# Kernel optimization log

Measured on AMD Instinct MI355X. Metric: run time of the kernel, lower is better.

Reference implementation:

```python
import jax, jax.numpy as jnp
import numpy as np

D_MODEL = 1024
N_HEADS = 16
D_KV = 64
INNER = N_HEADS * D_KV
NUM_BUCKETS = 32
MAX_DISTANCE = 128
B, S = 4, 2048


def _relative_position_bucket(relative_position):
    # Mirrors T5Attention._relative_position_bucket (bidirectional variant)
    num_buckets = NUM_BUCKETS // 2  # 16
    relative_buckets = (relative_position > 0).astype(jnp.int32) * num_buckets
    rp = jnp.abs(relative_position)
    max_exact = num_buckets // 2  # 8
    is_small = rp < max_exact
    # clamp to 1 before log to avoid -inf (masked out by where anyway)
    rp_large = max_exact + (
        jnp.log(jnp.maximum(rp, 1).astype(jnp.float32) / max_exact)
        / np.log(MAX_DISTANCE / max_exact)
        * (num_buckets - max_exact)
    ).astype(jnp.int32)
    rp_large = jnp.minimum(rp_large, num_buckets - 1)
    return relative_buckets + jnp.where(is_small, rp.astype(jnp.int32), rp_large)


def setup_inputs() -> dict:
    key = jax.random.key(0)
    k1, k2, k3, k4, k5, k6 = jax.random.split(key, 6)
    hidden_states = jax.random.normal(k1, (B, S, D_MODEL), dtype=jnp.float32)
    positions = jnp.arange(B * S, dtype=jnp.int64 if jax.config.jax_enable_x64 else jnp.int32).reshape(B, S)
    mask = jnp.ones((B, S), dtype=jnp.float32)
    sc = 1.0 / np.sqrt(D_MODEL)
    wq = jax.random.normal(k2, (INNER, D_MODEL), dtype=jnp.float32) * sc
    wk = jax.random.normal(k3, (INNER, D_MODEL), dtype=jnp.float32) * sc
    wv = jax.random.normal(k4, (INNER, D_MODEL), dtype=jnp.float32) * sc
    wo = jax.random.normal(k5, (D_MODEL, INNER), dtype=jnp.float32) * sc
    rel_bias = jax.random.normal(k6, (NUM_BUCKETS, N_HEADS), dtype=jnp.float32)
    return {"hidden_states": hidden_states, "positions": positions, "mask": mask,
            "wq": wq, "wk": wk, "wv": wv, "wo": wo, "rel_bias": rel_bias}


def reference(hidden_states, positions, mask, wq, wk, wv, wo, rel_bias):
    Bq, Sq, _ = hidden_states.shape

    def shape_heads(x):  # [B,S,inner] -> [B,H,S,dkv]
        return x.reshape(Bq, Sq, N_HEADS, D_KV).transpose(0, 2, 1, 3)

    # position bias: [B,H,Sq,Sk]
    rel_pos = positions[:, None, :] - positions[:, :, None]  # memory - context
    buckets = _relative_position_bucket(rel_pos)             # [B,Sq,Sk]
    position_bias = rel_bias[buckets].transpose(0, 3, 1, 2)  # [B,H,Sq,Sk]

    q = shape_heads(hidden_states @ wq.T).astype(jnp.float32)
    k = shape_heads(hidden_states @ wk.T).astype(jnp.float32)
    v = shape_heads(hidden_states @ wv.T).astype(jnp.float32)

    scores = jnp.einsum('bhqd,bhkd->bhqk', q, k)  # no 1/sqrt(d) scaling (T5)
    bias = position_bias - 1000.0 * (1.0 - mask[:, None, None, :])
    attn = jax.nn.softmax(scores + bias, axis=-1)  # dropout p=0

    ctx = jnp.einsum('bhqk,bhkd->bhqd', attn, v)
    ctx = ctx.transpose(0, 2, 1, 3).reshape(Bq, Sq, INNER).astype(hidden_states.dtype)
    return ctx @ wo.T
```

## Files before the change

kernel.cpp:

```cpp
#include <hip/hip_runtime.h>
#include <cstdint>
#include <cstddef>

#define D_MODEL 1024
#define N_HEADS 16
#define INNER   1024
#define NBATCH  4
#define SEQ     2048
#define MTOT    (NBATCH * SEQ)
#define LOG2E   1.44269504088896f
#define BSTRIDE 4352
#define MASKC   1442.695041f

typedef _Float16 f16;
typedef __attribute__((ext_vector_type(8))) _Float16 f16x8;
typedef __attribute__((ext_vector_type(4))) _Float16 f16x4;
typedef __attribute__((ext_vector_type(2))) _Float16 f16x2;
typedef __attribute__((ext_vector_type(2))) __fp16   h16x2;
typedef __attribute__((ext_vector_type(4))) float    f32x4;

__device__ __forceinline__ f16x2 cvtpk(float x, float y) {
#if __has_builtin(__builtin_amdgcn_cvt_pkrtz)
  h16x2 r = __builtin_amdgcn_cvt_pkrtz(x, y);
  return __builtin_bit_cast(f16x2, r);
#else
  f16x2 r; r[0] = (f16)x; r[1] = (f16)y; return r;
#endif
}
__device__ __forceinline__ float dot2acc(f16x2 p, float acc) {
#if __has_builtin(__builtin_amdgcn_fdot2)
  h16x2 a = __builtin_bit_cast(h16x2, p);
  h16x2 one; one[0] = (__fp16)1.0f; one[1] = (__fp16)1.0f;
  return __builtin_amdgcn_fdot2(a, one, acc, false);
#else
  return acc + (float)p[0] + (float)p[1];
#endif
}

__global__ void k_cvt(const float* __restrict__ src, f16* __restrict__ dst, int n4, float scale) {
  int i = blockIdx.x * 256 + threadIdx.x;
  if (i < n4) {
    const float4 v = reinterpret_cast<const float4*>(src)[i];
    f16x4 h;
    h[0] = (f16)(v.x * scale); h[1] = (f16)(v.y * scale);
    h[2] = (f16)(v.z * scale); h[3] = (f16)(v.w * scale);
    reinterpret_cast<f16x4*>(dst)[i] = h;
  }
}

__global__ void k_bias(const float* __restrict__ relb, float* __restrict__ biasG) {
  const int i = blockIdx.x * 256 + threadIdx.x;
  const int h = blockIdx.y;
  const int d = i - 2048;
  const int sgn = d > 0 ? 16 : 0;
  const int a = d < 0 ? -d : d;
  int bucket;
  if (a < 8) {
    bucket = a;
  } else {
    float t = logf((float)a / 8.0f);
    t = t / 2.772588722239781f;
    t = t * 8.0f;
    int lg = 8 + (int)t;
    bucket = lg < 15 ? lg : 15;
  }
  biasG[h * BSTRIDE + i] = relb[(sgn + bucket) * N_HEADS + h] * LOG2E - MASKC;
}

__device__ __forceinline__ void gload_lds16(const void* g, void* l) {
  __builtin_amdgcn_global_load_lds(
      (const __attribute__((address_space(1))) unsigned int*)g,
      (__attribute__((address_space(3))) unsigned int*)l,
      16, 0, 0);
}

template <int MODE>
__device__ __forceinline__ void gemm_body(const f16* __restrict__ A,
                                          const f16* __restrict__ W,
                                          void* __restrict__ Cp) {
  __shared__ __align__(16) f16 As[128 * 64];
  __shared__ __align__(16) f16 Bs[128 * 64];
  const int t = threadIdx.x;
  const int lane = t & 63;
  const int wid = t >> 6;
  const int wr = wid >> 1;
  const int wc = wid & 1;
  const int g = lane >> 4;
  const int lr = lane & 15;
  const int m0 = blockIdx.y * 128;
  const int n0 = blockIdx.x * 128;

  f32x4 acc[4][4] = {};
  const char* Ab = (const char*)A;
  const char* Wb = (const char*)W;

  for (int kt = 0; kt < D_MODEL / 64; ++kt) {
    const int k0 = kt * 64;
    __syncthreads();
#pragma unroll
    for (int i = 0; i < 4; ++i) {
      const int idx = i * 256 + t;
      const int row = idx >> 3;
      const int cb  = (idx & 7) * 16;
      gload_lds16(Ab + ((size_t)(m0 + row) * D_MODEL + k0) * 2 + cb, (char*)As + idx * 16);
      gload_lds16(Wb + ((size_t)(n0 + row) * D_MODEL + k0) * 2 + cb, (char*)Bs + idx * 16);
    }
    asm volatile("s_waitcnt vmcnt(0)" ::: "memory");
    __syncthreads();

    f16x8 af[4][2], bf[4][2];
#pragma unroll
    for (int mi = 0; mi < 4; ++mi)
#pragma unroll
      for (int kk = 0; kk < 2; ++kk)
        af[mi][kk] = *(const f16x8*)&As[(wr * 64 + mi * 16 + lr) * 64 + kk * 32 + g * 8];
#pragma unroll
    for (int ni = 0; ni < 4; ++ni)
#pragma unroll
      for (int kk = 0; kk < 2; ++kk)
        bf[ni][kk] = *(const f16x8*)&Bs[(wc * 64 + ni * 16 + lr) * 64 + kk * 32 + g * 8];
#pragma unroll
    for (int kk = 0; kk < 2; ++kk)
#pragma unroll
      for (int mi = 0; mi < 4; ++mi)
#pragma unroll
        for (int ni = 0; ni < 4; ++ni)
          acc[mi][ni] = __builtin_amdgcn_mfma_f32_16x16x32_f16(af[mi][kk], bf[ni][kk], acc[mi][ni], 0, 0, 0);
  }

#pragma unroll
  for (int mi = 0; mi < 4; ++mi)
#pragma unroll
    for (int ni = 0; ni < 4; ++ni) {
      const int n = n0 + wc * 64 + ni * 16 + lr;
      if (MODE == 2) {
        const int mbase = m0 + wr * 64 + mi * 16 + g * 4;
        const int b2 = mbase >> 11, s2 = mbase & (SEQ - 1);
        const int h2 = n >> 6, d2 = n & 63;
        f16x4 w;
#pragma unroll
        for (int r = 0; r < 4; ++r) w[r] = (f16)acc[mi][ni][r];
        *(f16x4*)((f16*)Cp + ((size_t)((b2 * 16 + h2) * 64 + d2) * SEQ + s2)) = w;
      } else {
#pragma unroll
        for (int r = 0; r < 4; ++r) {
          const int m = m0 + wr * 64 + mi * 16 + g * 4 + r;
          if (MODE == 1)
            ((float*)Cp)[(size_t)m * INNER + n] = acc[mi][ni][r];
          else
            ((f16*)Cp)[(size_t)m * INNER + n] = (f16)acc[mi][ni][r];
        }
      }
    }
}

__global__ __launch_bounds__(256) void k_gemm_qkv(
    const f16* __restrict__ A,
    const f16* __restrict__ Wq, const f16* __restrict__ Wk, const f16* __restrict__ Wv,
    f16* __restrict__ Cq, f16* __restrict__ Ck, f16* __restrict__ Vt) {
  if (blockIdx.z == 0)      gemm_body<0>(A, Wq, Cq);
  else if (blockIdx.z == 1) gemm_body<0>(A, Wk, Ck);
  else                      gemm_body<2>(A, Wv, Vt);
}

__global__ __launch_bounds__(256) void k_gemm_out(
    const f16* __restrict__ A, const f16* __restrict__ W, float* __restrict__ C) {
  gemm_body<1>(A, W, C);
}

__global__ __launch_bounds__(256, 4) void k_attn(
    const f16* __restrict__ Q, const f16* __restrict__ K, const f16* __restrict__ Vt,
    const float* __restrict__ biasG, const float* __restrict__ mask,
    f16* __restrict__ ctx) {
  __shared__ __align__(16) float biasT[2176];
  __shared__ __align__(16) f16 Ks[2 * 2048];
  __shared__ __align__(16) f16 Vs[2 * 2048];

  const int nb = (int)blockIdx.x;
  const int v = (nb & 7) * 128 + (nb >> 3);
  const int bh = v >> 4, qc = v & 15;
  const int b = bh >> 4, h = bh & 15;

  const int t = threadIdx.x, lane = t & 63, wid = t >> 6;
  const int g = lane >> 4, lr = lane & 15;
  const int qb = qc * 128;

  {
    const float* bgh = biasG + (size_t)h * BSTRIDE + (1921 - qb);
    for (int i = t; i < 2176; i += 256) biasT[i] = bgh[i];
  }

  const char* Kg = (const char*)K + ((size_t)(b * SEQ) * INNER + h * 64) * 2;
  const char* Vg = (const char*)Vt + ((size_t)bh * 64) * SEQ * 2;
  const float* maskB = mask + (size_t)b * SEQ;
  const int krow = t >> 3, kch = t & 7;
  const int ksrc = (kch * 16) ^ ((krow & 7) << 4);
  const int vrow = t >> 2, vch = t & 3;
  const int vsrc = (vch * 16) ^ ((vrow & 3) << 4);

  const int qw = qb + wid * 32;

  f16x8 qa[2][2];
#pragma unroll
  for (int hh = 0; hh < 2; ++hh)
#pragma unroll
    for (int kk = 0; kk < 2; ++kk)
      qa[hh][kk] = *(const f16x8*)&Q[(size_t)(b * SEQ + qw + hh * 16 + lr) * INNER + h * 64 + kk * 32 + g * 8];

  int koffs[2][2], voffs[2][4];
#pragma unroll
  for (int s = 0; s < 2; ++s) {
#pragma unroll
    for (int hf = 0; hf < 2; ++hf)
      koffs[s][hf] = (s * 16 + lr) * 128 + ((hf * 64 + g * 16) ^ ((lr & 7) << 4));
#pragma unroll
    for (int dn = 0; dn < 4; ++dn)
      voffs[s][dn] = (dn * 16 + lr) * 64 + ((s * 32 + g * 8) ^ ((lr & 3) << 4));
  }

  f32x4 o[2][4] = {};
  float mrun[2] = {-__builtin_inff(), -__builtin_inff()};
  float lsum[2] = {0.0f, 0.0f};
  const int jbase = 127 + 4 * g - wid * 32 - lr;

  gload_lds16(Kg + ((size_t)krow * INNER) * 2 + ksrc, (char*)Ks + t * 16);
  gload_lds16(Vg + ((size_t)vrow * SEQ) * 2 + vsrc,   (char*)Vs + t * 16);
  asm volatile("s_waitcnt vmcnt(0)" ::: "memory");
  __syncthreads();

#define ATTN_ITER(BUF, K0)                                                     \
  {                                                                            \
    const float4 mk0 = *(const float4*)(maskB + (K0) + 4 * g);                 \
    const float4 mk1 = *(const float4*)(maskB + (K0) + 16 + 4 * g);            \
    const int k0n_ = ((K0) + 32 < SEQ) ? (K0) + 32 : 0;                        \
    gload_lds16(Kg + ((size_t)(k0n_ + krow) * INNER) * 2 + ksrc,               \
                (char*)Ks + ((BUF) ^ 1) * 4096 + t * 16);                      \
    gload_lds16(Vg + ((size_t)vrow * SEQ + k0n_) * 2 + vsrc,                   \
                (char*)Vs + ((BUF) ^ 1) * 4096 + t * 16);                      \
    f16x8 kf[2][2];                                                            \
    _Pragma("unroll") for (int s = 0; s < 2; ++s)                              \
      _Pragma("unroll") for (int hf = 0; hf < 2; ++hf)                         \
        kf[s][hf] = *(const f16x8*)((const char*)Ks + (BUF) * 4096 + koffs[s][hf]); \
    f16x4 vf[2][4];                                                            \
    _Pragma("unroll") for (int s = 0; s < 2; ++s)                              \
      _Pragma("unroll") for (int dn = 0; dn < 4; ++dn)                         \
        vf[s][dn] = *(const f16x4*)((const char*)Vs + (BUF) * 4096 + voffs[s][dn]); \
    f32x4 sg[2][2];                                                            \
    _Pragma("unroll") for (int hh = 0; hh < 2; ++hh)                           \
      _Pragma("unroll") for (int s = 0; s < 2; ++s) {                          \
        const int jA = (K0) + s * 16 + jbase - hh * 16;                        \
        const float* mkp = (s == 0) ? (const float*)&mk0 : (const float*)&mk1; \
        f32x4 z;                                                               \
        _Pragma("unroll") for (int r = 0; r < 4; ++r)                          \
          z[r] = fmaf(mkp[r], MASKC, biasT[jA + r]);                           \
        z = __builtin_amdgcn_mfma_f32_16x16x32_f16(kf[s][0], qa[hh][0], z, 0, 0, 0); \
        z = __builtin_amdgcn_mfma_f32_16x16x32_f16(kf[s][1], qa[hh][1], z, 0, 0, 0); \
        sg[hh][s] = z;                                                         \
      }                                                                        \
    float mxA = fmaxf(fmaxf(fmaxf(sg[0][0][0], sg[0][0][1]), fmaxf(sg[0][0][2], sg[0][0][3])), \
                      fmaxf(fmaxf(sg[0][1][0], sg[0][1][1]), fmaxf(sg[0][1][2], sg[0][1][3]))); \
    float mxB = fmaxf(fmaxf(fmaxf(sg[1][0][0], sg[1][0][1]), fmaxf(sg[1][0][2], sg[1][0][3])), \
                      fmaxf(fmaxf(sg[1][1][0], sg[1][1][1]), fmaxf(sg[1][1][2], sg[1][1][3]))); \
    if (__any((mxA > mrun[0] + 11.5415603f) || (mxB > mrun[1] + 11.5415603f))) { \
      mxA = fmaxf(mxA, __shfl_xor(mxA, 16));                                   \
      mxB = fmaxf(mxB, __shfl_xor(mxB, 16));                                   \
      mxA = fmaxf(mxA, __shfl_xor(mxA, 32));                                   \
      mxB = fmaxf(mxB, __shfl_xor(mxB, 32));                                   \
      const float mnA = fmaxf(mrun[0], mxA), mnB = fmaxf(mrun[1], mxB);        \
      const float aA = __builtin_amdgcn_exp2f(mrun[0] - mnA);                  \
      const float aB = __builtin_amdgcn_exp2f(mrun[1] - mnB);                  \
      lsum[0] *= aA; lsum[1] *= aB;                                            \
      _Pragma("unroll") for (int dn = 0; dn < 4; ++dn)                         \
        _Pragma("unroll") for (int r = 0; r < 4; ++r) {                        \
          o[0][dn][r] *= aA; o[1][dn][r] *= aB;                                \
        }                                                                      \
      mrun[0] = mnA; mrun[1] = mnB;                                            \
    }                                                                          \
    f16x4 pfA[2], pfB[2];                                                      \
    _Pragma("unroll") for (int s = 0; s < 2; ++s) {                            \
      float eA[4], eB[4];                                                      \
      _Pragma("unroll") for (int r = 0; r < 4; ++r) {                          \
        eA[r] = __builtin_amdgcn_exp2f(sg[0][s][r] - mrun[0]);                 \
        eB[r] = __builtin_amdgcn_exp2f(sg[1][s][r] - mrun[1]);                 \
      }                                                                        \
      const f16x2 a0 = cvtpk(eA[0], eA[1]), a1 = cvtpk(eA[2], eA[3]);          \
      const f16x2 b0 = cvtpk(eB[0], eB[1]), b1 = cvtpk(eB[2], eB[3]);          \
      lsum[0] = dot2acc(a0, lsum[0]); lsum[0] = dot2acc(a1, lsum[0]);          \
      lsum[1] = dot2acc(b0, lsum[1]); lsum[1] = dot2acc(b1, lsum[1]);          \
      pfA[s][0] = a0[0]; pfA[s][1] = a0[1]; pfA[s][2] = a1[0]; pfA[s][3] = a1[1]; \
      pfB[s][0] = b0[0]; pfB[s][1] = b0[1]; pfB[s][2] = b1[0]; pfB[s][3] = b1[1]; \
    }                                                                          \
    _Pragma("unroll") for (int s = 0; s < 2; ++s)                              \
      _Pragma("unroll") for (int dn = 0; dn < 4; ++dn) {                       \
        o[0][dn] = __builtin_amdgcn_mfma_f32_16x16x16f16(vf[s][dn], pfA[s], o[0][dn], 0, 0, 0); \
        o[1][dn] = __builtin_amdgcn_mfma_f32_16x16x16f16(vf[s][dn], pfB[s], o[1][dn], 0, 0, 0); \
      }                                                                        \
    asm volatile("s_waitcnt vmcnt(0)" ::: "memory");                           \
    __syncthreads();                                                           \
  }

  for (int k0 = 0; k0 < SEQ; k0 += 64) {
    ATTN_ITER(0, k0)
    ATTN_ITER(1, k0 + 32)
  }

  lsum[0] += __shfl_xor(lsum[0], 16);
  lsum[1] += __shfl_xor(lsum[1], 16);
  lsum[0] += __shfl_xor(lsum[0], 32);
  lsum[1] += __shfl_xor(lsum[1], 32);

  const float invA = 1.0f / lsum[0], invB = 1.0f / lsum[1];
#pragma unroll
  for (int dn = 0; dn < 4; ++dn) {
    f16x4 wA, wB;
#pragma unroll
    for (int r = 0; r < 4; ++r) {
      wA[r] = (f16)(o[0][dn][r] * invA);
      wB[r] = (f16)(o[1][dn][r] * invB);
    }
    *(f16x4*)&ctx[(size_t)(b * SEQ + qw + lr) * INNER + h * 64 + dn * 16 + 4 * g] = wA;
    *(f16x4*)&ctx[(size_t)(b * SEQ + qw + 16 + lr) * INNER + h * 64 + dn * 16 + 4 * g] = wB;
  }
}

extern "C" void kernel_launch(void* const* d_in, const int* in_sizes, int n_in,
                              void* d_out, int out_size, void* d_ws, size_t ws_size,
                              hipStream_t stream) {
  const float* hs   = (const float*)d_in[0];
  const float* mask = (const float*)d_in[2];
  const float* wq   = (const float*)d_in[3];
  const float* wk   = (const float*)d_in[4];
  const float* wv   = (const float*)d_in[5];
  const float* wo   = (const float*)d_in[6];
  const float* relb = (const float*)d_in[7];

  char* ws = (char*)d_ws;
  const size_t SZ16 = (size_t)MTOT * INNER * 2;
  const size_t WSZ  = (size_t)INNER * D_MODEL * 2;
  f16* hs16 = (f16*)(ws);
  f16* q16  = (f16*)(ws + SZ16);
  f16* k16  = (f16*)(ws + 2 * SZ16);
  f16* vt16 = (f16*)(ws + 3 * SZ16);
  f16* wq16 = (f16*)(ws + 4 * SZ16);
  f16* wk16 = (f16*)(ws + 4 * SZ16 + WSZ);
  f16* wv16 = (f16*)(ws + 4 * SZ16 + 2 * WSZ);
  f16* wo16 = (f16*)(ws + 4 * SZ16 + 3 * WSZ);
  float* biasG = (float*)(ws + 4 * SZ16 + 4 * WSZ);

  k_cvt<<<(MTOT * INNER / 4 + 255) / 256, 256, 0, stream>>>(hs, hs16, MTOT * INNER / 4, 1.0f);
  k_cvt<<<(INNER * D_MODEL / 4 + 255) / 256, 256, 0, stream>>>(wq, wq16, INNER * D_MODEL / 4, LOG2E);
  k_cvt<<<(INNER * D_MODEL / 4 + 255) / 256, 256, 0, stream>>>(wk, wk16, INNER * D_MODEL / 4, 1.0f);
  k_cvt<<<(INNER * D_MODEL / 4 + 255) / 256, 256, 0, stream>>>(wv, wv16, INNER * D_MODEL / 4, 1.0f);
  k_cvt<<<(INNER * D_MODEL / 4 + 255) / 256, 256, 0, stream>>>(wo, wo16, INNER * D_MODEL / 4, 1.0f);

  k_bias<<<dim3(BSTRIDE / 256, N_HEADS), 256, 0, stream>>>(relb, biasG);

  k_gemm_qkv<<<dim3(INNER / 128, MTOT / 128, 3), 256, 0, stream>>>(
      hs16, wq16, wk16, wv16, q16, k16, vt16);

  k_attn<<<dim3(1024), 256, 0, stream>>>(
      q16, k16, vt16, biasG, mask, hs16);

  k_gemm_out<<<dim3(D_MODEL / 128, MTOT / 128), 256, 0, stream>>>(
      hs16, wo16, (float*)d_out);
}
```

Baseline: 255.1 us.

## Split attention work to 8 waves of 16 query rows each per block

Measured after the change: 309.5 us. 1.21x slower.

```diff
diff --git a/kernel.cpp b/kernel.cpp
--- a/kernel.cpp
+++ b/kernel.cpp
@@ -168,7 +168,7 @@
   gemm_body<1>(A, W, C);
 }
 
-__global__ __launch_bounds__(256, 4) void k_attn(
+__global__ __launch_bounds__(512, 6) void k_attn(
     const f16* __restrict__ Q, const f16* __restrict__ K, const f16* __restrict__ Vt,
     const float* __restrict__ biasG, const float* __restrict__ mask,
     f16* __restrict__ ctx) {
@@ -187,25 +187,26 @@
 
   {
     const float* bgh = biasG + (size_t)h * BSTRIDE + (1921 - qb);
-    for (int i = t; i < 2176; i += 256) biasT[i] = bgh[i];
+    for (int i = t; i < 2176; i += 512) biasT[i] = bgh[i];
   }
 
   const char* Kg = (const char*)K + ((size_t)(b * SEQ) * INNER + h * 64) * 2;
   const char* Vg = (const char*)Vt + ((size_t)bh * 64) * SEQ * 2;
   const float* maskB = mask + (size_t)b * SEQ;
-  const int krow = t >> 3, kch = t & 7;
-  const int ksrc = (kch * 16) ^ ((krow & 7) << 4);
-  const int vrow = t >> 2, vch = t & 3;
-  const int vsrc = (vch * 16) ^ ((vrow & 3) << 4);
-
-  const int qw = qb + wid * 32;
-
-  f16x8 qa[2][2];
-#pragma unroll
-  for (int hh = 0; hh < 2; ++hh)
-#pragma unroll
-    for (int kk = 0; kk < 2; ++kk)
-      qa[hh][kk] = *(const f16x8*)&Q[(size_t)(b * SEQ + qw + hh * 16 + lr) * INNER + h * 64 + kk * 32 + g * 8];
+
+  const bool isK = t < 256;
+  const int ts = t & 255;
+  const int krow = ts >> 3, kch = ts & 7;
+  const int vrow = ts >> 2, vch = ts & 3;
+  const int stsrc = isK ? ((kch * 16) ^ ((krow & 7) << 4))
+                        : ((vch * 16) ^ ((vrow & 3) << 4));
+
+  const int qw = qb + wid * 16;
+
+  f16x8 qa[2];
+#pragma unroll
+  for (int kk = 0; kk < 2; ++kk)
+    qa[kk] = *(const f16x8*)&Q[(size_t)(b * SEQ + qw + lr) * INNER + h * 64 + kk * 32 + g * 8];
 
   int koffs[2][2], voffs[2][4];
 #pragma unroll
@@ -218,13 +219,15 @@
       voffs[s][dn] = (dn * 16 + lr) * 64 + ((s * 32 + g * 8) ^ ((lr & 3) << 4));
   }
 
-  f32x4 o[2][4] = {};
-  float mrun[2] = {-__builtin_inff(), -__builtin_inff()};
-  float lsum[2] = {0.0f, 0.0f};
-  const int jbase = 127 + 4 * g - wid * 32 - lr;
-
-  gload_lds16(Kg + ((size_t)krow * INNER) * 2 + ksrc, (char*)Ks + t * 16);
-  gload_lds16(Vg + ((size_t)vrow * SEQ) * 2 + vsrc,   (char*)Vs + t * 16);
+  f32x4 o[4] = {};
+  float mrun = -__builtin_inff();
+  float lsum = 0.0f;
+  const int jbase = 127 + 4 * g - wid * 16 - lr;
+
+  if (isK)
+    gload_lds16(Kg + ((size_t)krow * INNER) * 2 + stsrc, (char*)Ks + ts * 16);
+  else
+    gload_lds16(Vg + ((size_t)vrow * SEQ) * 2 + stsrc,   (char*)Vs + ts * 16);
   asm volatile("s_waitcnt vmcnt(0)" ::: "memory");
   __syncthreads();
 
@@ -233,67 +236,53 @@
     const float4 mk0 = *(const float4*)(maskB + (K0) + 4 * g);                 \
     const float4 mk1 = *(const float4*)(maskB + (K0) + 16 + 4 * g);            \
     const int k0n_ = ((K0) + 32 < SEQ) ? (K0) + 32 : 0;                        \
-    gload_lds16(Kg + ((size_t)(k0n_ + krow) * INNER) * 2 + ksrc,               \
-                (char*)Ks + ((BUF) ^ 1) * 4096 + t * 16);                      \
-    gload_lds16(Vg + ((size_t)vrow * SEQ + k0n_) * 2 + vsrc,                   \
-                (char*)Vs + ((BUF) ^ 1) * 4096 + t * 16);                      \
+    if (isK)                                                                   \
+      gload_lds16(Kg + ((size_t)(k0n_ + krow) * INNER) * 2 + stsrc,            \
+                  (char*)Ks + ((BUF) ^ 1) * 4096 + ts * 16);                   \
+    else                                                                       \
+      gload_lds16(Vg + ((size_t)vrow * SEQ + k0n_) * 2 + stsrc,                \
+                  (char*)Vs + ((BUF) ^ 1) * 4096 + ts * 16);                   \
     f16x8 kf[2][2];                                                            \
     _Pragma("unroll") for (int s = 0; s < 2; ++s)                              \
       _Pragma("unroll") for (int hf = 0; hf < 2; ++hf)                         \
         kf[s][hf] = *(const f16x8*)((const char*)Ks + (BUF) * 4096 + koffs[s][hf]); \
-    f16x4 vf[2][4];                                                            \
-    _Pragma("unroll") for (int s = 0; s < 2; ++s)                              \
+    f32x4 sg[2];                                                               \
+    _Pragma("unroll") for (int s = 0; s < 2; ++s) {                            \
+      const int jA = (K0) + s * 16 + jbase;                                    \
+      const float* mkp = (s == 0) ? (const float*)&mk0 : (const float*)&mk1;   \
+      f32x4 z;                                                                 \
+      _Pragma("unroll") for (int r = 0; r < 4; ++r)                            \
+        z[r] = fmaf(mkp[r], MASKC, biasT[jA + r]);                             \
+      z = __builtin_amdgcn_mfma_f32_16x16x32_f16(kf[s][0], qa[0], z, 0, 0, 0); \
+      z = __builtin_amdgcn_mfma_f32_16x16x32_f16(kf[s][1], qa[1], z, 0, 0, 0); \
+      sg[s] = z;                                                               \
+    }                                                                          \
+    float mx = fmaxf(fmaxf(fmaxf(sg[0][0], sg[0][1]), fmaxf(sg[0][2], sg[0][3])), \
+                     fmaxf(fmaxf(sg[1][0], sg[1][1]), fmaxf(sg[1][2], sg[1][3]))); \
+    if (__any(mx > mrun + 11.5415603f)) {                                      \
+      mx = fmaxf(mx, __shfl_xor(mx, 16));                                      \
+      mx = fmaxf(mx, __shfl_xor(mx, 32));                                      \
+      const float mn = fmaxf(mrun, mx);                                        \
+      const float aA = __builtin_amdgcn_exp2f(mrun - mn);                      \
+      lsum *= aA;                                                              \
       _Pragma("unroll") for (int dn = 0; dn < 4; ++dn)                         \
-        vf[s][dn] = *(const f16x4*)((const char*)Vs + (BUF) * 4096 + voffs[s][dn]); \
-    f32x4 sg[2][2];                                                            \
-    _Pragma("unroll") for (int hh = 0; hh < 2; ++hh)                           \
-      _Pragma("unroll") for (int s = 0; s < 2; ++s) {                          \
-        const int jA = (K0) + s * 16 + jbase - hh * 16;                        \
-        const float* mkp = (s == 0) ? (const float*)&mk0 : (const float*)&mk1; \
-        f32x4 z;                                                               \
-        _Pragma("unroll") for (int r = 0; r < 4; ++r)                          \
-          z[r] = fmaf(mkp[r], MASKC, biasT[jA + r]);                           \
-        z = __builtin_amdgcn_mfma_f32_16x16x32_f16(kf[s][0], qa[hh][0], z, 0, 0, 0); \
-        z = __builtin_amdgcn_mfma_f32_16x16x32_f16(kf[s][1], qa[hh][1], z, 0, 0, 0); \
-        sg[hh][s] = z;                                                         \
-      }                                                                        \
-    float mxA = fmaxf(fmaxf(fmaxf(sg[0][0][0], sg[0][0][1]), fmaxf(sg[0][0][2], sg[0][0][3])), \
-                      fmaxf(fmaxf(sg[0][1][0], sg[0][1][1]), fmaxf(sg[0][1][2], sg[0][1][3]))); \
-    float mxB = fmaxf(fmaxf(fmaxf(sg[1][0][0], sg[1][0][1]), fmaxf(sg[1][0][2], sg[1][0][3])), \
-                      fmaxf(fmaxf(sg[1][1][0], sg[1][1][1]), fmaxf(sg[1][1][2], sg[1][1][3]))); \
-    if (__any((mxA > mrun[0] + 11.5415603f) || (mxB > mrun[1] + 11.5415603f))) { \
-      mxA = fmaxf(mxA, __shfl_xor(mxA, 16));                                   \
-      mxB = fmaxf(mxB, __shfl_xor(mxB, 16));                                   \
-      mxA = fmaxf(mxA, __shfl_xor(mxA, 32));                                   \
-      mxB = fmaxf(mxB, __shfl_xor(mxB, 32));                                   \
-      const float mnA = fmaxf(mrun[0], mxA), mnB = fmaxf(mrun[1], mxB);        \
-      const float aA = __builtin_amdgcn_exp2f(mrun[0] - mnA);                  \
-      const float aB = __builtin_amdgcn_exp2f(mrun[1] - mnB);                  \
-      lsum[0] *= aA; lsum[1] *= aB;                                            \
-      _Pragma("unroll") for (int dn = 0; dn < 4; ++dn)                         \
-        _Pragma("unroll") for (int r = 0; r < 4; ++r) {                        \
-          o[0][dn][r] *= aA; o[1][dn][r] *= aB;                                \
-        }                                                                      \
-      mrun[0] = mnA; mrun[1] = mnB;                                            \
+        _Pragma("unroll") for (int r = 0; r < 4; ++r) o[dn][r] *= aA;          \
+      mrun = mn;                                                               \
     }                                                                          \
-    f16x4 pfA[2], pfB[2];                                                      \
+    f16x4 pf[2];                                                               \
     _Pragma("unroll") for (int s = 0; s < 2; ++s) {                            \
-      float eA[4], eB[4];                                                      \
-      _Pragma("unroll") for (int r = 0; r < 4; ++r) {                          \
-        eA[r] = __builtin_amdgcn_exp2f(sg[0][s][r] - mrun[0]);                 \
-        eB[r] = __builtin_amdgcn_exp2f(sg[1][s][r] - mrun[1]);                 \
-      }                                                                        \
-      const f16x2 a0 = cvtpk(eA[0], eA[1]), a1 = cvtpk(eA[2], eA[3]);          \
-      const f16x2 b0 = cvtpk(eB[0], eB[1]), b1 = cvtpk(eB[2], eB[3]);          \
-      lsum[0] = dot2acc(a0, lsum[0]); lsum[0] = dot2acc(a1, lsum[0]);          \
-      lsum[1] = dot2acc(b0, lsum[1]); lsum[1] = dot2acc(b1, lsum[1]);          \
-      pfA[s][0] = a0[0]; pfA[s][1] = a0[1]; pfA[s][2] = a1[0]; pfA[s][3] = a1[1]; \
-      pfB[s][0] = b0[0]; pfB[s][1] = b0[1]; pfB[s][2] = b1[0]; pfB[s][3] = b1[1]; \
+      float e0 = __builtin_amdgcn_exp2f(sg[s][0] - mrun);                      \
+      float e1 = __builtin_amdgcn_exp2f(sg[s][1] - mrun);                      \
+      float e2 = __builtin_amdgcn_exp2f(sg[s][2] - mrun);                      \
+      float e3 = __builtin_amdgcn_exp2f(sg[s][3] - mrun);                      \
+      const f16x2 a0 = cvtpk(e0, e1), a1 = cvtpk(e2, e3);                      \
+      lsum = dot2acc(a0, lsum); lsum = dot2acc(a1, lsum);                      \
+      pf[s][0] = a0[0]; pf[s][1] = a0[1]; pf[s][2] = a1[0]; pf[s][3] = a1[1];  \
     }                                                                          \
     _Pragma("unroll") for (int s = 0; s < 2; ++s)                              \
       _Pragma("unroll") for (int dn = 0; dn < 4; ++dn) {                       \
-        o[0][dn] = __builtin_amdgcn_mfma_f32_16x16x16f16(vf[s][dn], pfA[s], o[0][dn], 0, 0, 0); \
-        o[1][dn] = __builtin_amdgcn_mfma_f32_16x16x16f16(vf[s][dn], pfB[s], o[1][dn], 0, 0, 0); \
+        const f16x4 vf = *(const f16x4*)((const char*)Vs + (BUF) * 4096 + voffs[s][dn]); \
+        o[dn] = __builtin_amdgcn_mfma_f32_16x16x16f16(vf, pf[s], o[dn], 0, 0, 0); \
       }                                                                        \
     asm volatile("s_waitcnt vmcnt(0)" ::: "memory");                           \
     __syncthreads();                                                           \
@@ -304,22 +293,16 @@
     ATTN_ITER(1, k0 + 32)
   }
 
-  lsum[0] += __shfl_xor(lsum[0], 16);
-  lsum[1] += __shfl_xor(lsum[1], 16);
-  lsum[0] += __shfl_xor(lsum[0], 32);
-  lsum[1] += __shfl_xor(lsum[1], 32);
-
-  const float invA = 1.0f / lsum[0], invB = 1.0f / lsum[1];
+  lsum += __shfl_xor(lsum, 16);
+  lsum += __shfl_xor(lsum, 32);
+
+  const float inv = 1.0f / lsum;
 #pragma unroll
   for (int dn = 0; dn < 4; ++dn) {
-    f16x4 wA, wB;
-#pragma unroll
-    for (int r = 0; r < 4; ++r) {
-      wA[r] = (f16)(o[0][dn][r] * invA);
-      wB[r] = (f16)(o[1][dn][r] * invB);
-    }
-    *(f16x4*)&ctx[(size_t)(b * SEQ + qw + lr) * INNER + h * 64 + dn * 16 + 4 * g] = wA;
-    *(f16x4*)&ctx[(size_t)(b * SEQ + qw + 16 + lr) * INNER + h * 64 + dn * 16 + 4 * g] = wB;
+    f16x4 w;
+#pragma unroll
+    for (int r = 0; r < 4; ++r) w[r] = (f16)(o[dn][r] * inv);
+    *(f16x4*)&ctx[(size_t)(b * SEQ + qw + lr) * INNER + h * 64 + dn * 16 + 4 * g] = w;
   }
 }
 
@@ -358,7 +341,7 @@
   k_gemm_qkv<<<dim3(INNER / 128, MTOT / 128, 3), 256, 0, stream>>>(
       hs16, wq16, wk16, wv16, q16, k16, vt16);
 
-  k_attn<<<dim3(1024), 256, 0, stream>>>(
+  k_attn<<<dim3(1024), 512, 0, stream>>>(
       q16, k16, vt16, biasG, mask, hs16);
 
   k_gemm_out<<<dim3(D_MODEL / 128, MTOT / 128), 256, 0, stream>>>(
```
